# Kernel tuning notes

Hardware: AMD Instinct MI355X
Metric: run time of the kernel (lower is better)

The kernel has to match this reference:

```python
import jax, jax.numpy as jnp
import numpy as np

N_NODES = 100000
M_EDGES = 500000
D = 128
L = 2
LRELU_SLOPE = 0.01
LN_EPS = 1e-5


def layer_norm(x, g, b):
    mu = jnp.mean(x, axis=-1, keepdims=True)
    var = jnp.var(x, axis=-1, keepdims=True)
    return (x - mu) * jax.lax.rsqrt(var + LN_EPS) * g + b


def leaky_relu(x):
    return jnp.where(x >= 0, x, LRELU_SLOPE * x)


def setup_inputs() -> dict:
    key = jax.random.key(0)
    ks = jax.random.split(key, 12)
    s = 1.0 / np.sqrt(D)
    inp = {
        "H": jax.random.normal(ks[0], (N_NODES, D), jnp.float32),
        "E": jax.random.normal(ks[1], (M_EDGES, D), jnp.float32),
        "ht": jax.random.randint(ks[2], (M_EDGES, 2), 0, N_NODES, jnp.int64) if jax.config.jax_enable_x64 else jax.random.randint(ks[2], (M_EDGES, 2), 0, N_NODES).astype(jnp.int32),
        "queries": jax.random.randint(ks[3], (M_EDGES,), 0, 2).astype(jnp.int32),
        # per-layer params stacked on leading L axis
        "W_eu": jax.random.uniform(ks[4], (L, 3 * D, D), jnp.float32, -s, s),
        "b_eu": jnp.zeros((L, D), jnp.float32),
        "ln_e_g": jnp.ones((L, D), jnp.float32),
        "ln_e_b": jnp.zeros((L, D), jnp.float32),
        "W_fwd": jax.random.uniform(ks[5], (L, 2 * D, D), jnp.float32, -s, s),
        "b_fwd": jnp.zeros((L, D), jnp.float32),
        "W_back": jax.random.uniform(ks[6], (L, 2 * D, D), jnp.float32, -s, s),
        "b_back": jnp.zeros((L, D), jnp.float32),
        "ln_h_g": jnp.ones((L, D), jnp.float32),
        "ln_h_b": jnp.zeros((L, D), jnp.float32),
    }
    return inp


def aggregate_messages(ht, messages_fwd, messages_back, n):
    # destinations: fwd msgs go to tails, back msgs go to heads
    msg_dst = jnp.concatenate([ht[:, 1], ht[:, 0]])  # [2m]
    messages = jnp.concatenate([messages_fwd, messages_back], axis=0)  # [2m, d]
    agg = jax.ops.segment_sum(messages, msg_dst, num_segments=n)  # [n, d]
    counts = jax.ops.segment_sum(jnp.ones_like(msg_dst, jnp.float32), msg_dst, num_segments=n)
    # torch yields nan/inf for count-0 nodes; clamp to 1 (0/1 = 0) for stability
    return agg / jnp.maximum(counts, 1.0)[:, None]


def reference(H, E, ht, queries, W_eu, b_eu, ln_e_g, ln_e_b,
              W_fwd, b_fwd, W_back, b_back, ln_h_g, ln_h_b):
    n = H.shape[0]
    for l in range(L):
        # --- EdgeUpdateLayer ---
        head_rep = H[ht[:, 0]]  # [m, d]
        tail_rep = H[ht[:, 1]]  # [m, d]
        triple = jnp.concatenate([head_rep, E, tail_rep], axis=1)  # [m, 3d]
        eu = leaky_relu(triple @ W_eu[l] + b_eu[l])
        E = layer_norm(eu + E, ln_e_g[l], ln_e_b[l])
        # --- MessagePassingLayer ---
        msgs_fwd = jnp.concatenate([H[ht[:, 0]], E], axis=1) @ W_fwd[l] + b_fwd[l]
        msgs_back = jnp.concatenate([H[ht[:, 1]], E], axis=1) @ W_back[l] + b_back[l]
        agg = aggregate_messages(ht, msgs_fwd, msgs_back, n)
        H = layer_norm(leaky_relu(agg) + H, ln_h_g[l], ln_h_b[l])
    return H
```

## Files before the change

### kernel.cpp

```cpp
#include <hip/hip_runtime.h>

#define N_NODES 100000
#define M_EDGES 500000
#define D 128
#define SLOPE 0.01f
#define EPS 1e-5f

typedef __attribute__((ext_vector_type(8))) short bf16x8;
typedef __attribute__((ext_vector_type(4))) float f32x4;
typedef __attribute__((ext_vector_type(4))) unsigned int u32x4;

__device__ __forceinline__ unsigned short f2bf(float f) {
    union { float f; unsigned u; } v; v.f = f;
    unsigned r = v.u + 0x7FFF + ((v.u >> 16) & 1);
    return (unsigned short)(r >> 16);
}
__device__ __forceinline__ float bf2f(unsigned short u) {
    union { unsigned u; float f; } v; v.u = ((unsigned)u) << 16; return v.f;
}
__device__ __forceinline__ u32x4 pack8v(f32x4 a, f32x4 b) {
    u32x4 r;
    r.x = ((unsigned)f2bf(a.y) << 16) | f2bf(a.x);
    r.y = ((unsigned)f2bf(a.w) << 16) | f2bf(a.z);
    r.z = ((unsigned)f2bf(b.y) << 16) | f2bf(b.x);
    r.w = ((unsigned)f2bf(b.w) << 16) | f2bf(b.z);
    return r;
}
#define GXT(v, nt) bf2f((unsigned short)(((nt) & 1) ? ((v)[(nt) >> 1] >> 16) : ((v)[(nt) >> 1] & 0xffff)))

__global__ void wconv_kernel(const float* __restrict__ src, unsigned short* __restrict__ dst,
                             int K, int total)
{
    int i = blockIdx.x * 256 + threadIdx.x;
    if (i >= total) return;
    int layer_sz = K * 128;
    int l = i / layer_sz;
    int r = i - l * layer_sz;
    int j    = r & 7;
    int lane = (r >> 3) & 63;
    int nt   = (r >> 9) & 7;
    int kk   = r >> 12;
    int row  = kk * 32 + ((lane >> 4) << 3) + j;
    int col  = nt * 16 + (lane & 15);
    dst[i] = f2bf(src[(size_t)l * layer_sz + row * 128 + col]);
}

__global__ void h2b_kernel(const float* __restrict__ src, unsigned short* __restrict__ dst, int total8)
{
    int i = blockIdx.x * 256 + threadIdx.x;
    if (i >= total8) return;
    f32x4 a = ((const f32x4*)src)[2 * i];
    f32x4 b = ((const f32x4*)src)[2 * i + 1];
    ((u32x4*)dst)[i] = pack8v(a, b);
}

__global__ void count_kernel(const int* __restrict__ ht, int* __restrict__ cnt, int m)
{
    int e = blockIdx.x * 256 + threadIdx.x;
    if (e < m) {
        atomicAdd(&cnt[ht[2 * e]],     1);
        atomicAdd(&cnt[ht[2 * e + 1]], 1);
    }
}

__global__ void scanA_kernel(const int* __restrict__ cnt, int* __restrict__ partial,
                             int* __restrict__ bsum, int n)
{
    __shared__ int tmp[256];
    int t = threadIdx.x, i = blockIdx.x * 256 + t;
    int v = (i < n) ? cnt[i] : 0;
    tmp[t] = v;
    __syncthreads();
    for (int s = 1; s < 256; s <<= 1) {
        int x = (t >= s) ? tmp[t - s] : 0;
        __syncthreads();
        tmp[t] += x;
        __syncthreads();
    }
    if (i < n) partial[i] = tmp[t] - v;
    if (t == 255) bsum[blockIdx.x] = tmp[255];
}

__global__ void scanB_kernel(int* __restrict__ bsum, int nb)
{
    __shared__ int tmp[512];
    int t = threadIdx.x;
    int v = (t < nb) ? bsum[t] : 0;
    tmp[t] = v;
    __syncthreads();
    for (int s = 1; s < 512; s <<= 1) {
        int x = (t >= s) ? tmp[t - s] : 0;
        __syncthreads();
        tmp[t] += x;
        __syncthreads();
    }
    if (t < nb) bsum[t] = tmp[t] - v;
}

__global__ void scanC_kernel(const int* __restrict__ partial, const int* __restrict__ bsum,
                             int* __restrict__ off, int* __restrict__ pos, int n)
{
    int i = blockIdx.x * 256 + threadIdx.x;
    if (i < n) {
        int o = partial[i] + bsum[blockIdx.x];
        off[i] = o;
        pos[i] = o;
    }
    if (i == 0) off[n] = 2 * M_EDGES;
}

__global__ void fill_kernel(const int* __restrict__ ht, int* __restrict__ pos,
                            int* __restrict__ slotF, int* __restrict__ slotB, int m)
{
    int e = blockIdx.x * 256 + threadIdx.x;
    if (e < m) {
        int2 p = ((const int2*)ht)[e];
        slotF[e] = atomicAdd(&pos[p.y], 1);
        slotB[e] = atomicAdd(&pos[p.x], 1);
    }
}

__global__ __launch_bounds__(256, 2)
void hw_kernel(const unsigned short* __restrict__ Hb,
               const unsigned short* __restrict__ B0,
               const unsigned short* __restrict__ B1,
               const unsigned short* __restrict__ B2,
               const unsigned short* __restrict__ B3,
               unsigned short* __restrict__ HW)
{
    __shared__ unsigned short bsh[16384];

    const int tid = threadIdx.x;
    const int wv  = tid >> 6;
    const int ln  = tid & 63;
    const int g   = ln >> 4;
    const int c15 = ln & 15;
    const int mb  = blockIdx.x >> 2;
    const int grp = blockIdx.x & 3;

    const unsigned short* Bsel = (grp == 0) ? B0 : (grp == 1) ? B1 : (grp == 2) ? B2 : B3;

    {
        const u32x4* bs = (const u32x4*)Bsel;
        u32x4* bd = (u32x4*)bsh;
#pragma unroll
        for (int it = 0; it < 8; ++it) bd[it * 256 + tid] = bs[it * 256 + tid];
    }

    const int rb = mb * 128 + wv * 32;
    const unsigned short* arow[2];
#pragma unroll
    for (int m = 0; m < 2; ++m) {
        int r = rb + m * 16 + c15;
        if (r >= N_NODES) r = N_NODES - 1;
        arow[m] = Hb + (size_t)r * 128;
    }
    __syncthreads();

    f32x4 acc[2][8];
#pragma unroll
    for (int m = 0; m < 2; ++m)
#pragma unroll
        for (int nt = 0; nt < 8; ++nt) acc[m][nt] = (f32x4){0.f, 0.f, 0.f, 0.f};

    __builtin_amdgcn_s_setprio(1);
#pragma unroll
    for (int kk = 0; kk < 4; ++kk) {
        bf16x8 a[2];
#pragma unroll
        for (int m = 0; m < 2; ++m) a[m] = *(const bf16x8*)(arow[m] + kk * 32 + g * 8);
#pragma unroll
        for (int nt = 0; nt < 8; ++nt) {
            bf16x8 b = *(const bf16x8*)(bsh + (kk * 8 + nt) * 512 + ln * 8);
#pragma unroll
            for (int m = 0; m < 2; ++m)
                acc[m][nt] = __builtin_amdgcn_mfma_f32_16x16x32_bf16(a[m], b, acc[m][nt], 0, 0, 0);
        }
    }
    __builtin_amdgcn_s_setprio(0);

#pragma unroll
    for (int m = 0; m < 2; ++m) {
#pragma unroll
        for (int rr = 0; rr < 4; ++rr) {
            int rg = rb + m * 16 + g * 4 + rr;
            if (rg < N_NODES) {
                u32x4 o;
                o.x = ((unsigned)f2bf(acc[m][1][rr]) << 16) | f2bf(acc[m][0][rr]);
                o.y = ((unsigned)f2bf(acc[m][3][rr]) << 16) | f2bf(acc[m][2][rr]);
                o.z = ((unsigned)f2bf(acc[m][5][rr]) << 16) | f2bf(acc[m][4][rr]);
                o.w = ((unsigned)f2bf(acc[m][7][rr]) << 16) | f2bf(acc[m][6][rr]);
                *(u32x4*)(HW + (size_t)rg * 512 + grp * 128 + c15 * 8) = o;
            }
        }
    }
}

template <bool E_F32, bool WRITE_E>
__global__ __launch_bounds__(64, 2)
void edge_mfma_kernel(const unsigned short* __restrict__ HW,
                      const float* __restrict__ E0,
                      const unsigned short* __restrict__ Ebf,
                      unsigned short* __restrict__ Eout,
                      const int* __restrict__ ht,
                      const unsigned short* __restrict__ Weu,
                      const unsigned short* __restrict__ Wf,
                      const unsigned short* __restrict__ Wb,
                      const float* __restrict__ beu,
                      const float* __restrict__ lneg, const float* __restrict__ lneb,
                      const float* __restrict__ bfw, const float* __restrict__ bbw,
                      const int* __restrict__ slotF, const int* __restrict__ slotB,
                      unsigned short* __restrict__ msg)
{
    __shared__ unsigned char en[8192];

    const int ln  = threadIdx.x;
    const int g   = ln >> 4;
    const int c15 = ln & 15;
    const int ew0 = blockIdx.x * 32;

    const int slotFv = slotF[ew0 + (ln & 31)];
    const int slotBv = slotB[ew0 + (ln & 31)];

    int hid[2][4], tln[2][4];
#pragma unroll
    for (int m = 0; m < 2; ++m)
#pragma unroll
        for (int rr = 0; rr < 4; ++rr) {
            int2 p = ((const int2*)ht)[ew0 + m * 16 + g * 4 + rr];
            hid[m][rr] = p.x;
            tln[m][rr] = p.y;
        }

    u32x4 ga[2][4], gc[2][4];
#pragma unroll
    for (int m = 0; m < 2; ++m)
#pragma unroll
        for (int rr = 0; rr < 4; ++rr) {
            ga[m][rr] = *(const u32x4*)(HW + (size_t)hid[m][rr] * 512 + c15 * 8);
            gc[m][rr] = *(const u32x4*)(HW + (size_t)tln[m][rr] * 512 + 128 + c15 * 8);
        }

#pragma unroll
    for (int it = 0; it < 8; ++it) {
        int lin = it * 1024 + ln * 16;
        int row = lin >> 8;
        int e   = ew0 + row;
        int elem = (lin & 255) >> 1;
        u32x4 pk;
        if (E_F32) {
            const float* s = E0 + (size_t)e * D + elem;
            pk = pack8v(*(const f32x4*)s, *(const f32x4*)(s + 4));
        } else {
            pk = *(const u32x4*)(Ebf + (size_t)e * D + elem);
        }
        *(u32x4*)(en + (lin ^ ((row & 7) << 4))) = pk;
    }

    const int ebase0 = c15 * 256 + g * 16;
    const int ebase1 = (16 + c15) * 256 + g * 16;
    const int swz    = (c15 & 7) << 4;

    f32x4 acc[2][8];

#pragma unroll
    for (int m = 0; m < 2; ++m)
#pragma unroll
        for (int nt = 0; nt < 8; ++nt) acc[m][nt] = (f32x4){0.f, 0.f, 0.f, 0.f};
    {
        const u32x4* Wg = (const u32x4*)Weu;
        u32x4 bc[8];
        bf16x8 a0, a1, a0n, a1n;
#pragma unroll
        for (int nt = 0; nt < 8; ++nt) bc[nt] = Wg[4 * 512 + nt * 64 + ln];
        a0 = *(const bf16x8*)(en + (ebase0 ^ swz));
        a1 = *(const bf16x8*)(en + (ebase1 ^ swz));
        __builtin_amdgcn_s_setprio(1);
#pragma unroll
        for (int kk = 0; kk < 4; ++kk) {
            if (kk < 3) {
                a0n = *(const bf16x8*)(en + ((ebase0 + (kk + 1) * 64) ^ swz));
                a1n = *(const bf16x8*)(en + ((ebase1 + (kk + 1) * 64) ^ swz));
            }
#pragma unroll
            for (int nt = 0; nt < 8; ++nt) {
                bf16x8 b = *(const bf16x8*)&bc[nt];
                acc[0][nt] = __builtin_amdgcn_mfma_f32_16x16x32_bf16(a0, b, acc[0][nt], 0, 0, 0);
                acc[1][nt] = __builtin_amdgcn_mfma_f32_16x16x32_bf16(a1, b, acc[1][nt], 0, 0, 0);
                if (kk < 3) bc[nt] = Wg[(5 + kk) * 512 + nt * 64 + ln];
            }
            a0 = a0n; a1 = a1n;
        }
        __builtin_amdgcn_s_setprio(0);
    }

    {
        float be[8], lg[8], lb[8];
#pragma unroll
        for (int nt = 0; nt < 8; ++nt) {
            be[nt] = beu[nt * 16 + c15];
            lg[nt] = lneg[nt * 16 + c15];
            lb[nt] = lneb[nt * 16 + c15];
        }
#pragma unroll
        for (int m = 0; m < 2; ++m) {
            float s[4] = {0.f,0.f,0.f,0.f}, ss[4] = {0.f,0.f,0.f,0.f};
#pragma unroll
            for (int nt = 0; nt < 8; ++nt) {
#pragma unroll
                for (int r = 0; r < 4; ++r) {
                    int row = m * 16 + g * 4 + r;
                    float x = acc[m][nt][r] + GXT(ga[m][r], nt) + GXT(gc[m][r], nt) + be[nt];
                    x = (x >= 0.f) ? x : SLOPE * x;
                    int lin = row * 256 + (nt * 16 + c15) * 2;
                    x += bf2f(*(const unsigned short*)(en + (lin ^ ((row & 7) << 4))));
                    acc[m][nt][r] = x;
                    s[r] += x; ss[r] += x * x;
                }
            }
#pragma unroll
            for (int d = 1; d < 16; d <<= 1) {
#pragma unroll
                for (int r = 0; r < 4; ++r) {
                    s[r]  += __shfl_xor(s[r],  d);
                    ss[r] += __shfl_xor(ss[r], d);
                }
            }
            float mu[4], rs[4];
#pragma unroll
            for (int r = 0; r < 4; ++r) {
                mu[r] = s[r] * (1.0f / 128.0f);
                float var = ss[r] * (1.0f / 128.0f) - mu[r] * mu[r];
                rs[r] = rsqrtf(var + EPS);
            }
#pragma unroll
            for (int nt = 0; nt < 8; ++nt) {
#pragma unroll
                for (int r = 0; r < 4; ++r) {
                    int row = m * 16 + g * 4 + r;
                    float xn = (acc[m][nt][r] - mu[r]) * rs[r] * lg[nt] + lb[nt];
                    int lin = row * 256 + (nt * 16 + c15) * 2;
                    *(unsigned short*)(en + (lin ^ ((row & 7) << 4))) = f2bf(xn);
                }
            }
        }
    }

    if (WRITE_E) {
#pragma unroll
        for (int it = 0; it < 8; ++it) {
            int lin = it * 1024 + ln * 16;
            int row = lin >> 8;
            *(u32x4*)(Eout + (size_t)(ew0 + row) * D + ((lin & 255) >> 1)) =
                *(const u32x4*)(en + (lin ^ ((row & 7) << 4)));
        }
    }

#pragma unroll 1
    for (int p = 0; p < 2; ++p) {
        const u32x4* Wg = (const u32x4*)(p ? Wb : Wf);
        const float* bias = p ? bbw : bfw;
        const int slotv = p ? slotBv : slotFv;

        u32x4 gm[2][4];
#pragma unroll
        for (int m = 0; m < 2; ++m)
#pragma unroll
            for (int rr = 0; rr < 4; ++rr) {
                int node = p ? tln[m][rr] : hid[m][rr];
                gm[m][rr] = *(const u32x4*)(HW + (size_t)node * 512 + 256 + p * 128 + c15 * 8);
            }

#pragma unroll
        for (int m = 0; m < 2; ++m)
#pragma unroll
            for (int nt = 0; nt < 8; ++nt) acc[m][nt] = (f32x4){0.f, 0.f, 0.f, 0.f};
        {
            u32x4 bc[8];
            bf16x8 a0, a1, a0n, a1n;
#pragma unroll
            for (int nt = 0; nt < 8; ++nt) bc[nt] = Wg[4 * 512 + nt * 64 + ln];
            a0 = *(const bf16x8*)(en + (ebase0 ^ swz));
            a1 = *(const bf16x8*)(en + (ebase1 ^ swz));
            __builtin_amdgcn_s_setprio(1);
#pragma unroll
            for (int kk = 0; kk < 4; ++kk) {
                if (kk < 3) {
                    a0n = *(const bf16x8*)(en + ((ebase0 + (kk + 1) * 64) ^ swz));
                    a1n = *(const bf16x8*)(en + ((ebase1 + (kk + 1) * 64) ^ swz));
                }
#pragma unroll
                for (int nt = 0; nt < 8; ++nt) {
                    bf16x8 b = *(const bf16x8*)&bc[nt];
                    acc[0][nt] = __builtin_amdgcn_mfma_f32_16x16x32_bf16(a0, b, acc[0][nt], 0, 0, 0);
                    acc[1][nt] = __builtin_amdgcn_mfma_f32_16x16x32_bf16(a1, b, acc[1][nt], 0, 0, 0);
                    if (kk < 3) bc[nt] = Wg[(5 + kk) * 512 + nt * 64 + ln];
                }
                a0 = a0n; a1 = a1n;
            }
            __builtin_amdgcn_s_setprio(0);
        }

        {
            float bv[8];
#pragma unroll
            for (int nt = 0; nt < 8; ++nt) bv[nt] = bias[nt * 16 + c15];
#pragma unroll
            for (int m = 0; m < 2; ++m) {
#pragma unroll
                for (int r = 0; r < 4; ++r) {
                    int erow = m * 16 + g * 4 + r;
                    int slot = __shfl(slotv, erow);
                    unsigned* base = (unsigned*)(msg + (size_t)slot * D + (c15 & ~1));
#pragma unroll
                    for (int nt = 0; nt < 8; ++nt) {
                        float v = acc[m][nt][r] + GXT(gm[m][r], nt) + bv[nt];
                        float o = __shfl_xor(v, 1);
                        float lo = (ln & 1) ? o : v;
                        float hi = (ln & 1) ? v : o;
                        unsigned pk = ((unsigned)f2bf(hi) << 16) | f2bf(lo);
                        if ((ln & 1) == (nt >> 2))
                            base[nt * 8] = pk;
                    }
                }
            }
        }
    }
}

__global__ __launch_bounds__(256)
void node_kernel(const float* __restrict__ Hin, const unsigned short* __restrict__ msg,
                 const int* __restrict__ off, const float* __restrict__ g,
                 const float* __restrict__ b, float* __restrict__ Hout,
                 unsigned short* __restrict__ Hb, int n)
{
    const int wave = threadIdx.x >> 6, lane = threadIdx.x & 63;
    const int node = blockIdx.x * 4 + wave;
    if (node >= n) return;

    const int beg = off[node], end = off[node + 1];
    const float inv = 1.0f / fmaxf((float)(end - beg), 1.0f);
    const unsigned* mb = (const unsigned*)msg;

    double a0 = 0., a1 = 0.;
    for (int i = beg; i < end; ++i) {
        unsigned v0 = mb[(size_t)i * 64 + lane];
        a0 += (double)bf2f((unsigned short)(v0 & 0xffff));
        a1 += (double)bf2f((unsigned short)(v0 >> 16));
    }

    float f0 = (float)a0 * inv;
    float f1 = (float)a1 * inv;
    f0 = (f0 >= 0.f) ? f0 : SLOPE * f0;
    f1 = (f1 >= 0.f) ? f1 : SLOPE * f1;

    size_t base = (size_t)node * D + 2 * lane;
    float x0 = f0 + Hin[base];
    float x1 = f1 + Hin[base + 1];

    float s = x0 + x1, ss = x0 * x0 + x1 * x1;
#pragma unroll
    for (int d = 1; d < 64; d <<= 1) {
        s  += __shfl_xor(s, d);
        ss += __shfl_xor(ss, d);
    }
    float mu  = s * (1.0f / 128.0f);
    float var = ss * (1.0f / 128.0f) - mu * mu;
    float rs  = rsqrtf(var + EPS);

    float o0 = (x0 - mu) * rs * g[2 * lane]     + b[2 * lane];
    float o1 = (x1 - mu) * rs * g[2 * lane + 1] + b[2 * lane + 1];
    Hout[base]     = o0;
    Hout[base + 1] = o1;
    Hb[base]       = f2bf(o0);
    Hb[base + 1]   = f2bf(o1);
}

extern "C" void kernel_launch(void* const* d_in, const int* in_sizes, int n_in,
                              void* d_out, int out_size, void* d_ws, size_t ws_size,
                              hipStream_t stream)
{
    const float* H0   = (const float*)d_in[0];
    const float* E0   = (const float*)d_in[1];
    const int*   ht   = (const int*)d_in[2];
    const float* Weu  = (const float*)d_in[4];
    const float* beu  = (const float*)d_in[5];
    const float* lneg = (const float*)d_in[6];
    const float* lneb = (const float*)d_in[7];
    const float* Wf   = (const float*)d_in[8];
    const float* bfw  = (const float*)d_in[9];
    const float* Wb   = (const float*)d_in[10];
    const float* bbw  = (const float*)d_in[11];
    const float* lnhg = (const float*)d_in[12];
    const float* lnhb = (const float*)d_in[13];

    float* Hout = (float*)d_out;

    char* ws = (char*)d_ws;
    unsigned short* msg    = (unsigned short*)(ws);
    unsigned short* Ebuf   = (unsigned short*)(ws + 256000000);
    unsigned short* HW     = (unsigned short*)(ws + 384000000);
    unsigned short* Hb     = (unsigned short*)(ws + 486400000);
    unsigned short* Weu_sw = (unsigned short*)(ws + 512000000);
    unsigned short* Wf_sw  = (unsigned short*)(ws + 512196608);
    unsigned short* Wb_sw  = (unsigned short*)(ws + 512327680);
    int*            cnt    = (int*)(ws + 512458752);
    int*            partial= (int*)(ws + 512858752);
    int*            bsum   = (int*)(ws + 513258752);
    int*            off    = (int*)(ws + 513260800);
    int*            pos    = (int*)(ws + 513660816);
    int*            slotF  = (int*)(ws + 514060816);
    int*            slotB  = (int*)(ws + 516060816);

    wconv_kernel<<<(2*384*128 + 255)/256, 256, 0, stream>>>(Weu, Weu_sw, 384, 2*384*128);
    wconv_kernel<<<(2*256*128 + 255)/256, 256, 0, stream>>>(Wf,  Wf_sw,  256, 2*256*128);
    wconv_kernel<<<(2*256*128 + 255)/256, 256, 0, stream>>>(Wb,  Wb_sw,  256, 2*256*128);
    h2b_kernel<<<(N_NODES * D / 8 + 255)/256, 256, 0, stream>>>(H0, Hb, N_NODES * D / 8);

    const int nscan = (N_NODES + 255) / 256;
    hipMemsetAsync(cnt, 0, (size_t)N_NODES * sizeof(int), stream);
    count_kernel<<<(M_EDGES + 255) / 256, 256, 0, stream>>>(ht, cnt, M_EDGES);
    scanA_kernel<<<nscan, 256, 0, stream>>>(cnt, partial, bsum, N_NODES);
    scanB_kernel<<<1, 512, 0, stream>>>(bsum, nscan);
    scanC_kernel<<<nscan, 256, 0, stream>>>(partial, bsum, off, pos, N_NODES);
    fill_kernel<<<(M_EDGES + 255) / 256, 256, 0, stream>>>(ht, pos, slotF, slotB, M_EDGES);

    const int hwblocks = ((N_NODES + 127) / 128) * 4;
    const int eblocks  = M_EDGES / 32;

    for (int l = 0; l < 2; ++l) {
        const float* Hin = (l == 0) ? H0 : Hout;
        const unsigned short* WeuL = Weu_sw + (size_t)l * 49152;
        const unsigned short* WfL  = Wf_sw  + (size_t)l * 32768;
        const unsigned short* WbL  = Wb_sw  + (size_t)l * 32768;

        hw_kernel<<<hwblocks, 256, 0, stream>>>(
            Hb, WeuL, WeuL + 8 * 4096, WfL, WbL, HW);

        if (l == 0) {
            edge_mfma_kernel<true, true><<<eblocks, 64, 0, stream>>>(
                HW, E0, nullptr, Ebuf, ht, WeuL, WfL, WbL,
                beu, lneg, lneb, bfw, bbw, slotF, slotB, msg);
        } else {
            edge_mfma_kernel<false, false><<<eblocks, 64, 0, stream>>>(
                HW, nullptr, Ebuf, nullptr, ht, WeuL, WfL, WbL,
                beu + D, lneg + D, lneb + D, bfw + D, bbw + D, slotF, slotB, msg);
        }

        node_kernel<<<(N_NODES + 3) / 4, 256, 0, stream>>>(
            Hin, msg, off, lnhg + (size_t)l * D, lnhb + (size_t)l * D, Hout, Hb, N_NODES);
    }
}
```

Baseline: 975.1 us.

## Shrink edge kernel tile to 16 edges per wave and unroll node aggregation

The edge MFMA kernel now processes 16 edges per 64-thread block instead of 32, which halves the accumulator, gather-register and LDS footprint and raises the launch-bounds occupancy hint from 2 to 3. The node kernel's segment-sum loop is unrolled by two with independent double accumulators to expose more memory-level parallelism. The s_setprio hints are removed from both the hw and edge kernels. In exchange, each weight-fragment load is reused over fewer edge rows, so global and L2 traffic for the weights doubles, and twice as many blocks are launched.

Result: faster. 925.0 us (-5.1%).

```diff
diff --git a/kernel.cpp b/kernel.cpp
--- a/kernel.cpp
+++ b/kernel.cpp
@@ -163,7 +163,6 @@
 #pragma unroll
         for (int nt = 0; nt < 8; ++nt) acc[m][nt] = (f32x4){0.f, 0.f, 0.f, 0.f};
 
-    __builtin_amdgcn_s_setprio(1);
 #pragma unroll
     for (int kk = 0; kk < 4; ++kk) {
         bf16x8 a[2];
@@ -177,7 +176,6 @@
                 acc[m][nt] = __builtin_amdgcn_mfma_f32_16x16x32_bf16(a[m], b, acc[m][nt], 0, 0, 0);
         }
     }
-    __builtin_amdgcn_s_setprio(0);
 
 #pragma unroll
     for (int m = 0; m < 2; ++m) {
@@ -197,7 +195,7 @@
 }
 
 template <bool E_F32, bool WRITE_E>
-__global__ __launch_bounds__(64, 2)
+__global__ __launch_bounds__(64, 3)
 void edge_mfma_kernel(const unsigned short* __restrict__ HW,
                       const float* __restrict__ E0,
                       const unsigned short* __restrict__ Ebf,
@@ -212,37 +210,33 @@
                       const int* __restrict__ slotF, const int* __restrict__ slotB,
                       unsigned short* __restrict__ msg)
 {
-    __shared__ unsigned char en[8192];
+    __shared__ unsigned char en[4096];
 
     const int ln  = threadIdx.x;
     const int g   = ln >> 4;
     const int c15 = ln & 15;
-    const int ew0 = blockIdx.x * 32;
-
-    const int slotFv = slotF[ew0 + (ln & 31)];
-    const int slotBv = slotB[ew0 + (ln & 31)];
-
-    int hid[2][4], tln[2][4];
-#pragma unroll
-    for (int m = 0; m < 2; ++m)
-#pragma unroll
-        for (int rr = 0; rr < 4; ++rr) {
-            int2 p = ((const int2*)ht)[ew0 + m * 16 + g * 4 + rr];
-            hid[m][rr] = p.x;
-            tln[m][rr] = p.y;
-        }
-
-    u32x4 ga[2][4], gc[2][4];
-#pragma unroll
-    for (int m = 0; m < 2; ++m)
-#pragma unroll
-        for (int rr = 0; rr < 4; ++rr) {
-            ga[m][rr] = *(const u32x4*)(HW + (size_t)hid[m][rr] * 512 + c15 * 8);
-            gc[m][rr] = *(const u32x4*)(HW + (size_t)tln[m][rr] * 512 + 128 + c15 * 8);
-        }
-
-#pragma unroll
-    for (int it = 0; it < 8; ++it) {
+    const int ew0 = blockIdx.x * 16;
+
+    const int slotFv = slotF[ew0 + c15];
+    const int slotBv = slotB[ew0 + c15];
+
+    int hid[4], tln_[4];
+#pragma unroll
+    for (int rr = 0; rr < 4; ++rr) {
+        int2 p = ((const int2*)ht)[ew0 + g * 4 + rr];
+        hid[rr]  = p.x;
+        tln_[rr] = p.y;
+    }
+
+    u32x4 ga[4], gc[4];
+#pragma unroll
+    for (int rr = 0; rr < 4; ++rr) {
+        ga[rr] = *(const u32x4*)(HW + (size_t)hid[rr]  * 512 + c15 * 8);
+        gc[rr] = *(const u32x4*)(HW + (size_t)tln_[rr] * 512 + 128 + c15 * 8);
+    }
+
+#pragma unroll
+    for (int it = 0; it < 4; ++it) {
         int lin = it * 1024 + ln * 16;
         int row = lin >> 8;
         int e   = ew0 + row;
@@ -257,41 +251,32 @@
         *(u32x4*)(en + (lin ^ ((row & 7) << 4))) = pk;
     }
 
-    const int ebase0 = c15 * 256 + g * 16;
-    const int ebase1 = (16 + c15) * 256 + g * 16;
-    const int swz    = (c15 & 7) << 4;
-
-    f32x4 acc[2][8];
-
-#pragma unroll
-    for (int m = 0; m < 2; ++m)
-#pragma unroll
-        for (int nt = 0; nt < 8; ++nt) acc[m][nt] = (f32x4){0.f, 0.f, 0.f, 0.f};
+    const int ebase = c15 * 256 + g * 16;
+    const int swz   = (c15 & 7) << 4;
+
+    f32x4 acc[8];
+
+#pragma unroll
+    for (int nt = 0; nt < 8; ++nt) acc[nt] = (f32x4){0.f, 0.f, 0.f, 0.f};
     {
         const u32x4* Wg = (const u32x4*)Weu;
         u32x4 bc[8];
-        bf16x8 a0, a1, a0n, a1n;
+        bf16x8 a0, a0n;
 #pragma unroll
         for (int nt = 0; nt < 8; ++nt) bc[nt] = Wg[4 * 512 + nt * 64 + ln];
-        a0 = *(const bf16x8*)(en + (ebase0 ^ swz));
-        a1 = *(const bf16x8*)(en + (ebase1 ^ swz));
-        __builtin_amdgcn_s_setprio(1);
+        a0 = *(const bf16x8*)(en + (ebase ^ swz));
 #pragma unroll
         for (int kk = 0; kk < 4; ++kk) {
-            if (kk < 3) {
-                a0n = *(const bf16x8*)(en + ((ebase0 + (kk + 1) * 64) ^ swz));
-                a1n = *(const bf16x8*)(en + ((ebase1 + (kk + 1) * 64) ^ swz));
-            }
+            if (kk < 3)
+                a0n = *(const bf16x8*)(en + ((ebase + (kk + 1) * 64) ^ swz));
 #pragma unroll
             for (int nt = 0; nt < 8; ++nt) {
                 bf16x8 b = *(const bf16x8*)&bc[nt];
-                acc[0][nt] = __builtin_amdgcn_mfma_f32_16x16x32_bf16(a0, b, acc[0][nt], 0, 0, 0);
-                acc[1][nt] = __builtin_amdgcn_mfma_f32_16x16x32_bf16(a1, b, acc[1][nt], 0, 0, 0);
+                acc[nt] = __builtin_amdgcn_mfma_f32_16x16x32_bf16(a0, b, acc[nt], 0, 0, 0);
                 if (kk < 3) bc[nt] = Wg[(5 + kk) * 512 + nt * 64 + ln];
             }
-            a0 = a0n; a1 = a1n;
-        }
-        __builtin_amdgcn_s_setprio(0);
+            a0 = a0n;
+        }
     }
 
     {
@@ -302,53 +287,50 @@
             lg[nt] = lneg[nt * 16 + c15];
             lb[nt] = lneb[nt * 16 + c15];
         }
-#pragma unroll
-        for (int m = 0; m < 2; ++m) {
-            float s[4] = {0.f,0.f,0.f,0.f}, ss[4] = {0.f,0.f,0.f,0.f};
-#pragma unroll
-            for (int nt = 0; nt < 8; ++nt) {
-#pragma unroll
-                for (int r = 0; r < 4; ++r) {
-                    int row = m * 16 + g * 4 + r;
-                    float x = acc[m][nt][r] + GXT(ga[m][r], nt) + GXT(gc[m][r], nt) + be[nt];
-                    x = (x >= 0.f) ? x : SLOPE * x;
-                    int lin = row * 256 + (nt * 16 + c15) * 2;
-                    x += bf2f(*(const unsigned short*)(en + (lin ^ ((row & 7) << 4))));
-                    acc[m][nt][r] = x;
-                    s[r] += x; ss[r] += x * x;
-                }
-            }
-#pragma unroll
-            for (int d = 1; d < 16; d <<= 1) {
-#pragma unroll
-                for (int r = 0; r < 4; ++r) {
-                    s[r]  += __shfl_xor(s[r],  d);
-                    ss[r] += __shfl_xor(ss[r], d);
-                }
-            }
-            float mu[4], rs[4];
+        float s[4] = {0.f,0.f,0.f,0.f}, ss[4] = {0.f,0.f,0.f,0.f};
+#pragma unroll
+        for (int nt = 0; nt < 8; ++nt) {
 #pragma unroll
             for (int r = 0; r < 4; ++r) {
-                mu[r] = s[r] * (1.0f / 128.0f);
-                float var = ss[r] * (1.0f / 128.0f) - mu[r] * mu[r];
-                rs[r] = rsqrtf(var + EPS);
-            }
-#pragma unroll
-            for (int nt = 0; nt < 8; ++nt) {
-#pragma unroll
-                for (int r = 0; r < 4; ++r) {
-                    int row = m * 16 + g * 4 + r;
-                    float xn = (acc[m][nt][r] - mu[r]) * rs[r] * lg[nt] + lb[nt];
-                    int lin = row * 256 + (nt * 16 + c15) * 2;
-                    *(unsigned short*)(en + (lin ^ ((row & 7) << 4))) = f2bf(xn);
-                }
+                int row = g * 4 + r;
+                float x = acc[nt][r] + GXT(ga[r], nt) + GXT(gc[r], nt) + be[nt];
+                x = (x >= 0.f) ? x : SLOPE * x;
+                int lin = row * 256 + (nt * 16 + c15) * 2;
+                x += bf2f(*(const unsigned short*)(en + (lin ^ ((row & 7) << 4))));
+                acc[nt][r] = x;
+                s[r] += x; ss[r] += x * x;
+            }
+        }
+#pragma unroll
+        for (int d = 1; d < 16; d <<= 1) {
+#pragma unroll
+            for (int r = 0; r < 4; ++r) {
+                s[r]  += __shfl_xor(s[r],  d);
+                ss[r] += __shfl_xor(ss[r], d);
+            }
+        }
+        float mu[4], rs[4];
+#pragma unroll
+        for (int r = 0; r < 4; ++r) {
+            mu[r] = s[r] * (1.0f / 128.0f);
+            float var = ss[r] * (1.0f / 128.0f) - mu[r] * mu[r];
+            rs[r] = rsqrtf(var + EPS);
+        }
+#pragma unroll
+        for (int nt = 0; nt < 8; ++nt) {
+#pragma unroll
+            for (int r = 0; r < 4; ++r) {
+                int row = g * 4 + r;
+                float xn = (acc[nt][r] - mu[r]) * rs[r] * lg[nt] + lb[nt];
+                int lin = row * 256 + (nt * 16 + c15) * 2;
+                *(unsigned short*)(en + (lin ^ ((row & 7) << 4))) = f2bf(xn);
             }
         }
     }
 
     if (WRITE_E) {
 #pragma unroll
-        for (int it = 0; it < 8; ++it) {
+        for (int it = 0; it < 4; ++it) {
             int lin = it * 1024 + ln * 16;
             int row = lin >> 8;
             *(u32x4*)(Eout + (size_t)(ew0 + row) * D + ((lin & 255) >> 1)) =
@@ -362,43 +344,33 @@
         const float* bias = p ? bbw : bfw;
         const int slotv = p ? slotBv : slotFv;
 
-        u32x4 gm[2][4];
-#pragma unroll
-        for (int m = 0; m < 2; ++m)
-#pragma unroll
-            for (int rr = 0; rr < 4; ++rr) {
-                int node = p ? tln[m][rr] : hid[m][rr];
-                gm[m][rr] = *(const u32x4*)(HW + (size_t)node * 512 + 256 + p * 128 + c15 * 8);
-            }
-
-#pragma unroll
-        for (int m = 0; m < 2; ++m)
-#pragma unroll
-            for (int nt = 0; nt < 8; ++nt) acc[m][nt] = (f32x4){0.f, 0.f, 0.f, 0.f};
+        u32x4 gm[4];
+#pragma unroll
+        for (int rr = 0; rr < 4; ++rr) {
+            int node = p ? tln_[rr] : hid[rr];
+            gm[rr] = *(const u32x4*)(HW + (size_t)node * 512 + 256 + p * 128 + c15 * 8);
+        }
+
+#pragma unroll
+        for (int nt = 0; nt < 8; ++nt) acc[nt] = (f32x4){0.f, 0.f, 0.f, 0.f};
         {
             u32x4 bc[8];
-            bf16x8 a0, a1, a0n, a1n;
+            bf16x8 a0, a0n;
 #pragma unroll
             for (int nt = 0; nt < 8; ++nt) bc[nt] = Wg[4 * 512 + nt * 64 + ln];
-            a0 = *(const bf16x8*)(en + (ebase0 ^ swz));
-            a1 = *(const bf16x8*)(en + (ebase1 ^ swz));
-            __builtin_amdgcn_s_setprio(1);
+            a0 = *(const bf16x8*)(en + (ebase ^ swz));
 #pragma unroll
             for (int kk = 0; kk < 4; ++kk) {
-                if (kk < 3) {
-                    a0n = *(const bf16x8*)(en + ((ebase0 + (kk + 1) * 64) ^ swz));
-                    a1n = *(const bf16x8*)(en + ((ebase1 + (kk + 1) * 64) ^ swz));
-                }
+                if (kk < 3)
+                    a0n = *(const bf16x8*)(en + ((ebase + (kk + 1) * 64) ^ swz));
 #pragma unroll
                 for (int nt = 0; nt < 8; ++nt) {
                     bf16x8 b = *(const bf16x8*)&bc[nt];
-                    acc[0][nt] = __builtin_amdgcn_mfma_f32_16x16x32_bf16(a0, b, acc[0][nt], 0, 0, 0);
-                    acc[1][nt] = __builtin_amdgcn_mfma_f32_16x16x32_bf16(a1, b, acc[1][nt], 0, 0, 0);
+                    acc[nt] = __builtin_amdgcn_mfma_f32_16x16x32_bf16(a0, b, acc[nt], 0, 0, 0);
                     if (kk < 3) bc[nt] = Wg[(5 + kk) * 512 + nt * 64 + ln];
                 }
-                a0 = a0n; a1 = a1n;
-            }
-            __builtin_amdgcn_s_setprio(0);
+                a0 = a0n;
+            }
         }
 
         {
@@ -406,22 +378,19 @@
 #pragma unroll
             for (int nt = 0; nt < 8; ++nt) bv[nt] = bias[nt * 16 + c15];
 #pragma unroll
-            for (int m = 0; m < 2; ++m) {
-#pragma unroll
-                for (int r = 0; r < 4; ++r) {
-                    int erow = m * 16 + g * 4 + r;
-                    int slot = __shfl(slotv, erow);
-                    unsigned* base = (unsigned*)(msg + (size_t)slot * D + (c15 & ~1));
-#pragma unroll
-                    for (int nt = 0; nt < 8; ++nt) {
-                        float v = acc[m][nt][r] + GXT(gm[m][r], nt) + bv[nt];
-                        float o = __shfl_xor(v, 1);
-                        float lo = (ln & 1) ? o : v;
-                        float hi = (ln & 1) ? v : o;
-                        unsigned pk = ((unsigned)f2bf(hi) << 16) | f2bf(lo);
-                        if ((ln & 1) == (nt >> 2))
-                            base[nt * 8] = pk;
-                    }
+            for (int r = 0; r < 4; ++r) {
+                int erow = g * 4 + r;
+                int slot = __shfl(slotv, erow);
+                unsigned* base = (unsigned*)(msg + (size_t)slot * D + (c15 & ~1));
+#pragma unroll
+                for (int nt = 0; nt < 8; ++nt) {
+                    float v = acc[nt][r] + GXT(gm[r], nt) + bv[nt];
+                    float o = __shfl_xor(v, 1);
+                    float lo = (ln & 1) ? o : v;
+                    float hi = (ln & 1) ? v : o;
+                    unsigned pk = ((unsigned)f2bf(hi) << 16) | f2bf(lo);
+                    if ((ln & 1) == (nt >> 2))
+                        base[nt * 8] = pk;
                 }
             }
         }
@@ -442,12 +411,22 @@
     const float inv = 1.0f / fmaxf((float)(end - beg), 1.0f);
     const unsigned* mb = (const unsigned*)msg;
 
-    double a0 = 0., a1 = 0.;
-    for (int i = beg; i < end; ++i) {
+    double a0 = 0., a1 = 0., b0 = 0., b1 = 0.;
+    int i = beg;
+    for (; i + 1 < end; i += 2) {
+        unsigned v0 = mb[(size_t)i * 64 + lane];
+        unsigned v1 = mb[(size_t)(i + 1) * 64 + lane];
+        a0 += (double)bf2f((unsigned short)(v0 & 0xffff));
+        a1 += (double)bf2f((unsigned short)(v0 >> 16));
+        b0 += (double)bf2f((unsigned short)(v1 & 0xffff));
+        b1 += (double)bf2f((unsigned short)(v1 >> 16));
+    }
+    if (i < end) {
         unsigned v0 = mb[(size_t)i * 64 + lane];
         a0 += (double)bf2f((unsigned short)(v0 & 0xffff));
         a1 += (double)bf2f((unsigned short)(v0 >> 16));
     }
+    a0 += b0; a1 += b1;
 
     float f0 = (float)a0 * inv;
     float f1 = (float)a1 * inv;
@@ -526,7 +505,7 @@
     fill_kernel<<<(M_EDGES + 255) / 256, 256, 0, stream>>>(ht, pos, slotF, slotB, M_EDGES);
 
     const int hwblocks = ((N_NODES + 127) / 128) * 4;
-    const int eblocks  = M_EDGES / 32;
+    const int eblocks  = M_EDGES / 16;
 
     for (int l = 0; l < 2; ++l) {
         const float* Hin = (l == 0) ? H0 : Hout;
```
